# Kernel optimization log

Hardware: AMD Instinct MI355X
Metric: run time of the kernel (lower is better)

## Reference

```python
import jax, jax.numpy as jnp
import numpy as np

B, N, F = 32, 64, 128          # batch, num_nodes, n_in_node
K, H, M, NH = 4, 256, 256, 256 # edge_types, msg_hid, msg_out, n_hid
E = N * (N - 1)                # fully-connected directed edges = 4032


def setup_inputs() -> dict:
    key = jax.random.key(0)
    ks = jax.random.split(key, 12)
    inputs = jax.random.normal(ks[0], (B, N, F), dtype=jnp.float32)
    # soft edge-type assignment per edge (rows sum to 1, as in NRI)
    rel_type = jax.nn.softmax(jax.random.normal(ks[1], (B, E, K), dtype=jnp.float32), axis=-1)
    # one-hot receiver/sender matrices for all i != j pairs
    idx = np.array([(i, j) for i in range(N) for j in range(N) if i != j], dtype=np.int64)
    eye = np.eye(N, dtype=np.float32)
    rel_rec = jnp.asarray(eye[idx[:, 0]])   # [E, N]
    rel_send = jnp.asarray(eye[idx[:, 1]])  # [E, N]
    # per-edge-type message MLP weights (stacked over K): y = x @ W + b
    W1 = jax.random.normal(ks[2], (K, 2 * F, H), dtype=jnp.float32) / np.sqrt(2 * F)
    b1 = jnp.zeros((K, H), dtype=jnp.float32)
    W2 = jax.random.normal(ks[3], (K, H, M), dtype=jnp.float32) / np.sqrt(H)
    b2 = jnp.zeros((K, M), dtype=jnp.float32)
    # output MLP
    Wo1 = jax.random.normal(ks[4], (F + M, NH), dtype=jnp.float32) / np.sqrt(F + M)
    bo1 = jnp.zeros((NH,), dtype=jnp.float32)
    Wo2 = jax.random.normal(ks[5], (NH, NH), dtype=jnp.float32) / np.sqrt(NH)
    bo2 = jnp.zeros((NH,), dtype=jnp.float32)
    Wo3 = jax.random.normal(ks[6], (NH, F), dtype=jnp.float32) / np.sqrt(NH)
    bo3 = jnp.zeros((F,), dtype=jnp.float32)
    return {"inputs": inputs, "rel_type": rel_type, "rel_rec": rel_rec, "rel_send": rel_send,
            "W1": W1, "b1": b1, "W2": W2, "b2": b2,
            "Wo1": Wo1, "bo1": bo1, "Wo2": Wo2, "bo2": bo2, "Wo3": Wo3, "bo3": bo3}


def reference(inputs, rel_type, rel_rec, rel_send, W1, b1, W2, b2, Wo1, bo1, Wo2, bo2, Wo3, bo3):
    # gather node states to edges via one-hot matmul (as in the source)
    receivers = jnp.einsum('en,bnf->bef', rel_rec, inputs)   # [B,E,F]
    senders = jnp.einsum('en,bnf->bef', rel_send, inputs)    # [B,E,F]
    pre_msg = jnp.concatenate([receivers, senders], axis=-1)  # [B,E,2F]
    # per-edge-type 2-layer ReLU MLP, batched over the K edge types
    h = jax.nn.relu(jnp.einsum('bef,kfh->bkeh', pre_msg, W1) + b1[:, None, :])  # [B,K,E,H]
    msg = jax.nn.relu(jnp.einsum('bkeh,khm->bkem', h, W2) + b2[:, None, :])     # [B,K,E,M]
    # mask by soft edge type and accumulate over types (dropout p=0 -> identity)
    all_msgs = jnp.einsum('bkem,bek->bem', msg, rel_type)     # [B,E,M]
    # scatter-aggregate messages to receiver nodes via one-hot matmul
    agg_msgs = jnp.einsum('en,bem->bnm', rel_rec, all_msgs)   # [B,N,M]
    aug = jnp.concatenate([inputs, agg_msgs], axis=-1)        # [B,N,F+M]
    p = jax.nn.relu(aug @ Wo1 + bo1)
    p = jax.nn.relu(p @ Wo2 + bo2)
    p = p @ Wo3 + bo3
    return inputs + p
```

## Files before the change

### kernel.cpp

```cpp
#include <hip/hip_runtime.h>


#define B_ 32
#define N_ 64
#define F_ 128
#define K_ 4
#define E_ 4032

#define WS_W2T 0u
#define WS_R   524288u
#define WS_S   4718592u
#define WS_AGG 8912896u

typedef unsigned short u16;
typedef u16    u16x4  __attribute__((ext_vector_type(4)));
typedef u16    u16x8  __attribute__((ext_vector_type(8)));
typedef __bf16 bf16x8 __attribute__((ext_vector_type(8)));
typedef float  f32x4  __attribute__((ext_vector_type(4)));
typedef float  f32x16 __attribute__((ext_vector_type(16)));

__device__ __forceinline__ u16 f2bf(float f) {
    unsigned u; __builtin_memcpy(&u, &f, 4);
    return (u16)((u + 0x7FFFu + ((u >> 16) & 1u)) >> 16);
}
__device__ __forceinline__ float bf2f(u16 u) {
    unsigned v = ((unsigned)u) << 16;
    float f; __builtin_memcpy(&f, &v, 4); return f;
}
__device__ __forceinline__ void gl_lds16(const u16* g, u16* l) {
    __builtin_amdgcn_global_load_lds(
        (const __attribute__((address_space(1))) void*)g,
        (__attribute__((address_space(3))) void*)l, 16, 0, 0);
}

#define LBAR() do { \
    asm volatile("s_waitcnt lgkmcnt(0)" ::: "memory"); \
    __builtin_amdgcn_s_barrier(); \
    __builtin_amdgcn_sched_barrier(0); \
} while (0)

__global__ __launch_bounds__(256) void prep_rs_kernel(
    const float* __restrict__ W2, const float* __restrict__ x,
    const float* __restrict__ W1, const float* __restrict__ b1,
    u16* __restrict__ W2t, u16* __restrict__ R, u16* __restrict__ S)
{
    __shared__ u16 ldsA[64 * 136];
    __shared__ u16 ldsW[32 * 136];
    const int tid = threadIdx.x;

    if (blockIdx.x < 1024) {
        unsigned gid = blockIdx.x * 256u + tid;
        unsigned chunk = gid >> 13, r = gid & 8191u;
        unsigned g = r >> 11, n = (r >> 3) & 255u, e = r & 7u;
        unsigned k = chunk >> 3, kc = chunk & 7u, ks2 = g >> 1, lhh = g & 1u;
        unsigned kk = kc * 32u + ks2 * 16u + lhh * 8u + e;
        W2t[gid] = f2bf(W2[(k * 256u + kk) * 256u + n]);
        return;
    }

    const int lane = tid & 63, w = tid >> 6;
    const int quad = lane >> 4, mloc = lane & 15;
    const int bx = blockIdx.x - 1024;
    const int k = bx >> 6, half = (bx >> 5) & 1, b = bx & 31;

    for (int idx = tid; idx < 2048; idx += 256) {
        int row = idx >> 5, c4 = idx & 31;
        f32x4 v = *(const f32x4*)&x[(b * 64 + row) * 128 + c4 * 4];
        u16x4 o;
#pragma unroll
        for (int e = 0; e < 4; ++e) o[e] = f2bf(v[e]);
        *(u16x4*)&ldsA[row * 136 + c4 * 4] = o;
    }
    __syncthreads();

    bf16x8 aF[4];
#pragma unroll
    for (int ks = 0; ks < 4; ++ks)
        aF[ks] = *(const bf16x8*)&ldsA[(w * 16 + mloc) * 136 + quad * 8 + ks * 32];

    u16* dst = half ? S : R;
    for (int c = 0; c < 8; ++c) {
        __syncthreads();
        for (int idx = tid; idx < 4096; idx += 256) {
            int n = idx & 31, f = idx >> 5;
            ldsW[n * 136 + f] = f2bf(W1[(k * 256 + half * 128 + f) * 256 + c * 32 + n]);
        }
        __syncthreads();
#pragma unroll
        for (int nt = 0; nt < 2; ++nt) {
            f32x4 acc = (f32x4){0.f, 0.f, 0.f, 0.f};
            const int boff = (nt * 16 + mloc) * 136 + quad * 8;
#pragma unroll
            for (int ks = 0; ks < 4; ++ks)
                acc = __builtin_amdgcn_mfma_f32_16x16x32_bf16(
                    aF[ks], *(const bf16x8*)&ldsW[boff + ks * 32], acc, 0, 0, 0);
            const int n = c * 32 + nt * 16 + mloc;
            const float bias = half ? 0.f : b1[k * 256 + n];
#pragma unroll
            for (int r = 0; r < 4; ++r) {
                int row = w * 16 + quad * 4 + r;
                if (half) {
                    dst[((size_t)((k * 8 + c) * 2048 + b * 64 + row)) * 32 + nt * 16 + mloc]
                        = f2bf(acc[r] + bias);
                } else {
                    dst[((size_t)(k * 2048 + b * 64 + row)) * 256 + n] = f2bf(acc[r] + bias);
                }
            }
        }
    }
}

__global__ __launch_bounds__(256, 3) void edge9_kernel(
    const u16* __restrict__ R, const u16* __restrict__ S2,
    const float* __restrict__ rel, const u16* __restrict__ W2t,
    const float* __restrict__ b2, u16* __restrict__ aggb)
{
    __shared__ u16   WtS[2][8192];
    __shared__ u16   HS[2][4][64][8];
    __shared__ float Rf[4][256];
    __shared__ float rtS[4][64];

    const int tid  = threadIdx.x;
    const int lane = tid & 63;
    const int w    = tid >> 6;
    const int l31  = lane & 31;
    const int lh   = lane >> 5;
    const int bid  = ((blockIdx.x & 7) << 8) | (blockIdx.x >> 3);
    const int b    = bid >> 6;
    const int i    = bid & 63;

    {
        const u16* src = W2t + w * 2048;
        u16* dst = &WtS[0][w * 2048];
#pragma unroll
        for (int it2 = 0; it2 < 4; ++it2)
            gl_lds16(src + it2 * 512 + lane * 8, dst + it2 * 512);
    }
    {
        const int k = tid >> 6, j = tid & 63;
        float v = 0.f;
        if (j != i) v = rel[((size_t)(b * E_) + i * 63 + (j - (j > i))) * 4 + k];
        rtS[k][j] = v;
    }
    {
        const int k = tid >> 6, e4 = tid & 63;
        u16x4 t4 = *(const u16x4*)&R[((size_t)(k * 2048 + b * 64 + i)) * 256 + e4 * 4];
#pragma unroll
        for (int e = 0; e < 4; ++e) Rf[k][e4 * 4 + e] = bf2f(t4[e]);
    }
    u16x8 sv = *(const u16x8*)&S2[((size_t)(b * 64 + lane)) * 32 + w * 8];
    __syncthreads();

    {
        const float* rp = &Rf[0][w * 8];
        f32x4 r0 = *(const f32x4*)rp, r1 = *(const f32x4*)(rp + 4);
        bf16x8 o;
#pragma unroll
        for (int e = 0; e < 4; ++e) {
            o[e]     = (__bf16)fmaxf(r0[e] + bf2f(sv[e]),     0.f);
            o[4 + e] = (__bf16)fmaxf(r1[e] + bf2f(sv[4 + e]), 0.f);
        }
        *(bf16x8*)&HS[0][w][lane][0] = o;
    }
    __syncthreads();

    float amsg[2] = {0.f, 0.f};
    f32x16 acc[2][2];

    for (int it = 0; it < 32; ++it) {
        const int kT = it >> 3, kcT = it & 7;
        if (kcT == 0) {
#pragma unroll
            for (int mt = 0; mt < 2; ++mt)
#pragma unroll
                for (int nt = 0; nt < 2; ++nt) acc[mt][nt] = (f32x16)(0.f);
        }
        u16x8 svN;
        if (it < 31) {
            svN = *(const u16x8*)&S2[((size_t)((it + 1) * 2048 + b * 64 + lane)) * 32 + w * 8];
            const u16* src = W2t + (size_t)(it + 1) * 8192 + w * 2048;
            u16* dst = &WtS[(it + 1) & 1][w * 2048];
#pragma unroll
            for (int it2 = 0; it2 < 4; ++it2)
                gl_lds16(src + it2 * 512 + lane * 8, dst + it2 * 512);
        }
        const u16* buf = WtS[it & 1];
        const u16(*hs)[64][8] = HS[it & 1];
#pragma unroll
        for (int ks2 = 0; ks2 < 2; ++ks2) {
            bf16x8 A0 = *(const bf16x8*)&hs[ks2 * 2 + lh][l31][0];
            bf16x8 A1 = *(const bf16x8*)&hs[ks2 * 2 + lh][32 + l31][0];
            bf16x8 B0 = *(const bf16x8*)&buf[(ks2 * 2 + lh) * 2048 + (w * 64 + l31) * 8];
            bf16x8 B1 = *(const bf16x8*)&buf[(ks2 * 2 + lh) * 2048 + (w * 64 + 32 + l31) * 8];
            acc[0][0] = __builtin_amdgcn_mfma_f32_32x32x16_bf16(A0, B0, acc[0][0], 0, 0, 0);
            acc[0][1] = __builtin_amdgcn_mfma_f32_32x32x16_bf16(A0, B1, acc[0][1], 0, 0, 0);
            acc[1][0] = __builtin_amdgcn_mfma_f32_32x32x16_bf16(A1, B0, acc[1][0], 0, 0, 0);
            acc[1][1] = __builtin_amdgcn_mfma_f32_32x32x16_bf16(A1, B1, acc[1][1], 0, 0, 0);
        }
        if (it < 31) {
            const int kT2 = (it + 1) >> 3, kc2 = (it + 1) & 7;
            const float* rp = &Rf[kT2][kc2 * 32 + w * 8];
            f32x4 r0 = *(const f32x4*)rp, r1 = *(const f32x4*)(rp + 4);
            bf16x8 o;
#pragma unroll
            for (int e = 0; e < 4; ++e) {
                o[e]     = (__bf16)fmaxf(r0[e] + bf2f(svN[e]),     0.f);
                o[4 + e] = (__bf16)fmaxf(r1[e] + bf2f(svN[4 + e]), 0.f);
            }
            *(bf16x8*)&HS[(it + 1) & 1][w][lane][0] = o;
        }
        if (kcT == 7) {
#pragma unroll
            for (int nt = 0; nt < 2; ++nt) {
                const float bias = b2[kT * 256 + w * 64 + nt * 32 + l31];
#pragma unroll
                for (int mt = 0; mt < 2; ++mt) {
                    float s = 0.f;
#pragma unroll
                    for (int rq = 0; rq < 4; ++rq) {
                        f32x4 rt4 = *(const f32x4*)&rtS[kT][mt * 32 + rq * 8 + 4 * lh];
#pragma unroll
                        for (int e = 0; e < 4; ++e) {
                            float v = acc[mt][nt][rq * 4 + e] + bias;
                            v = v > 0.f ? v : 0.f;
                            s += rt4[e] * v;
                        }
                    }
                    amsg[nt] += s;
                }
            }
        }
        __syncthreads();
    }

#pragma unroll
    for (int nt = 0; nt < 2; ++nt) {
        float s = amsg[nt] + __shfl_xor(amsg[nt], 32);
        if (lh == 0)
            aggb[(size_t)(b * 64 + i) * 256 + w * 64 + nt * 32 + l31] = f2bf(s);
    }
}

__global__ __launch_bounds__(256) void outmlp3_kernel(
    const float* __restrict__ x, const u16* __restrict__ aggb,
    const float* __restrict__ Wo1, const float* __restrict__ bo1,
    const float* __restrict__ Wo2, const float* __restrict__ bo2,
    const float* __restrict__ Wo3, const float* __restrict__ bo3,
    float* __restrict__ out)
{
    __shared__ u16 wch[4][256][8];
    __shared__ u16 p1S[32 * 264];
    __shared__ u16 p2S[32 * 264];
    const int tid = threadIdx.x, lane = tid & 63, w = tid >> 6;
    const int quad = lane >> 4, mloc = lane & 15;
    const int row0 = blockIdx.x * 32;

    {
        f32x4 acc[2][4];
#pragma unroll
        for (int mt = 0; mt < 2; ++mt)
#pragma unroll
            for (int nt = 0; nt < 4; ++nt) acc[mt][nt] = (f32x4){0.f, 0.f, 0.f, 0.f};
        float wr[32];
#pragma unroll
        for (int g = 0; g < 4; ++g)
#pragma unroll
            for (int e = 0; e < 8; ++e) wr[g * 8 + e] = Wo1[(g * 8 + e) * 256 + tid];
        for (int kk = 0; kk < 12; ++kk) {
            bf16x8 aF[2];
#pragma unroll
            for (int mt = 0; mt < 2; ++mt) {
                const int row = row0 + mt * 16 + mloc;
                if (kk < 4) {
                    u16x8 t;
#pragma unroll
                    for (int e = 0; e < 8; ++e) t[e] = f2bf(x[row * 128 + kk * 32 + quad * 8 + e]);
                    __builtin_memcpy(&aF[mt], &t, 16);
                } else {
                    aF[mt] = *(const bf16x8*)&aggb[(size_t)row * 256 + (kk - 4) * 32 + quad * 8];
                }
            }
#pragma unroll
            for (int g = 0; g < 4; ++g) {
                u16x8 o;
#pragma unroll
                for (int e = 0; e < 8; ++e) o[e] = f2bf(wr[g * 8 + e]);
                *(u16x8*)&wch[g][tid][0] = o;
            }
            if (kk + 1 < 12) {
#pragma unroll
                for (int g = 0; g < 4; ++g)
#pragma unroll
                    for (int e = 0; e < 8; ++e) wr[g * 8 + e] = Wo1[((kk + 1) * 32 + g * 8 + e) * 256 + tid];
            }
            LBAR();
#pragma unroll
            for (int nt = 0; nt < 4; ++nt) {
                bf16x8 bF = *(const bf16x8*)&wch[quad][w * 64 + nt * 16 + mloc][0];
#pragma unroll
                for (int mt = 0; mt < 2; ++mt)
                    acc[mt][nt] = __builtin_amdgcn_mfma_f32_16x16x32_bf16(aF[mt], bF, acc[mt][nt], 0, 0, 0);
            }
            LBAR();
        }
#pragma unroll
        for (int nt = 0; nt < 4; ++nt) {
            const int n = w * 64 + nt * 16 + mloc;
            const float bias = bo1[n];
#pragma unroll
            for (int mt = 0; mt < 2; ++mt)
#pragma unroll
                for (int r = 0; r < 4; ++r) {
                    float v = acc[mt][nt][r] + bias;
                    p1S[(mt * 16 + quad * 4 + r) * 264 + n] = f2bf(v > 0.f ? v : 0.f);
                }
        }
    }
    LBAR();
    {
        f32x4 acc[2][4];
#pragma unroll
        for (int mt = 0; mt < 2; ++mt)
#pragma unroll
            for (int nt = 0; nt < 4; ++nt) acc[mt][nt] = (f32x4){0.f, 0.f, 0.f, 0.f};
        float wr[32];
#pragma unroll
        for (int g = 0; g < 4; ++g)
#pragma unroll
            for (int e = 0; e < 8; ++e) wr[g * 8 + e] = Wo2[(g * 8 + e) * 256 + tid];
        for (int kk = 0; kk < 8; ++kk) {
            bf16x8 aF[2];
#pragma unroll
            for (int mt = 0; mt < 2; ++mt)
                aF[mt] = *(const bf16x8*)&p1S[(mt * 16 + mloc) * 264 + kk * 32 + quad * 8];
#pragma unroll
            for (int g = 0; g < 4; ++g) {
                u16x8 o;
#pragma unroll
                for (int e = 0; e < 8; ++e) o[e] = f2bf(wr[g * 8 + e]);
                *(u16x8*)&wch[g][tid][0] = o;
            }
            if (kk + 1 < 8) {
#pragma unroll
                for (int g = 0; g < 4; ++g)
#pragma unroll
                    for (int e = 0; e < 8; ++e) wr[g * 8 + e] = Wo2[((kk + 1) * 32 + g * 8 + e) * 256 + tid];
            }
            LBAR();
#pragma unroll
            for (int nt = 0; nt < 4; ++nt) {
                bf16x8 bF = *(const bf16x8*)&wch[quad][w * 64 + nt * 16 + mloc][0];
#pragma unroll
                for (int mt = 0; mt < 2; ++mt)
                    acc[mt][nt] = __builtin_amdgcn_mfma_f32_16x16x32_bf16(aF[mt], bF, acc[mt][nt], 0, 0, 0);
            }
            LBAR();
        }
#pragma unroll
        for (int nt = 0; nt < 4; ++nt) {
            const int n = w * 64 + nt * 16 + mloc;
            const float bias = bo2[n];
#pragma unroll
            for (int mt = 0; mt < 2; ++mt)
#pragma unroll
                for (int r = 0; r < 4; ++r) {
                    float v = acc[mt][nt][r] + bias;
                    p2S[(mt * 16 + quad * 4 + r) * 264 + n] = f2bf(v > 0.f ? v : 0.f);
                }
        }
    }
    LBAR();
    {
        f32x4 acc[2][2];
#pragma unroll
        for (int mt = 0; mt < 2; ++mt)
#pragma unroll
            for (int nt = 0; nt < 2; ++nt) acc[mt][nt] = (f32x4){0.f, 0.f, 0.f, 0.f};
        const int sn = tid & 127, sh = tid >> 7;
        float wr[16];
#pragma unroll
        for (int g2 = 0; g2 < 2; ++g2)
#pragma unroll
            for (int e = 0; e < 8; ++e) wr[g2 * 8 + e] = Wo3[((sh * 2 + g2) * 8 + e) * 128 + sn];
        for (int kk = 0; kk < 8; ++kk) {
            bf16x8 aF[2];
#pragma unroll
            for (int mt = 0; mt < 2; ++mt)
                aF[mt] = *(const bf16x8*)&p2S[(mt * 16 + mloc) * 264 + kk * 32 + quad * 8];
#pragma unroll
            for (int g2 = 0; g2 < 2; ++g2) {
                const int g = sh * 2 + g2;
                u16x8 o;
#pragma unroll
                for (int e = 0; e < 8; ++e) o[e] = f2bf(wr[g2 * 8 + e]);
                *(u16x8*)&wch[g][sn][0] = o;
            }
            if (kk + 1 < 8) {
#pragma unroll
                for (int g2 = 0; g2 < 2; ++g2)
#pragma unroll
                    for (int e = 0; e < 8; ++e)
                        wr[g2 * 8 + e] = Wo3[((kk + 1) * 32 + (sh * 2 + g2) * 8 + e) * 128 + sn];
            }
            LBAR();
#pragma unroll
            for (int nt = 0; nt < 2; ++nt) {
                bf16x8 bF = *(const bf16x8*)&wch[quad][w * 32 + nt * 16 + mloc][0];
#pragma unroll
                for (int mt = 0; mt < 2; ++mt)
                    acc[mt][nt] = __builtin_amdgcn_mfma_f32_16x16x32_bf16(aF[mt], bF, acc[mt][nt], 0, 0, 0);
            }
            LBAR();
        }
#pragma unroll
        for (int nt = 0; nt < 2; ++nt) {
            const int n = w * 32 + nt * 16 + mloc;
            const float bias = bo3[n];
#pragma unroll
            for (int mt = 0; mt < 2; ++mt)
#pragma unroll
                for (int r = 0; r < 4; ++r) {
                    const int grow = row0 + mt * 16 + quad * 4 + r;
                    out[grow * 128 + n] = x[grow * 128 + n] + acc[mt][nt][r] + bias;
                }
        }
    }
}

extern "C" void kernel_launch(void* const* d_in, const int* in_sizes, int n_in,
                              void* d_out, int out_size, void* d_ws, size_t ws_size,
                              hipStream_t stream) {
    const float* x   = (const float*)d_in[0];
    const float* rel = (const float*)d_in[1];
    const float* W1  = (const float*)d_in[4];
    const float* b1  = (const float*)d_in[5];
    const float* W2  = (const float*)d_in[6];
    const float* b2  = (const float*)d_in[7];
    const float* Wo1 = (const float*)d_in[8];
    const float* bo1 = (const float*)d_in[9];
    const float* Wo2 = (const float*)d_in[10];
    const float* bo2 = (const float*)d_in[11];
    const float* Wo3 = (const float*)d_in[12];
    const float* bo3 = (const float*)d_in[13];
    float* out = (float*)d_out;

    char* ws = (char*)d_ws;
    u16* W2t  = (u16*)(ws + WS_W2T);
    u16* R    = (u16*)(ws + WS_R);
    u16* S2   = (u16*)(ws + WS_S);
    u16* aggb = (u16*)(ws + WS_AGG);

    prep_rs_kernel<<<1280, 256, 0, stream>>>(W2, x, W1, b1, W2t, R, S2);
    edge9_kernel<<<2048, 256, 0, stream>>>(R, S2, rel, W2t, b2, aggb);
    outmlp3_kernel<<<64, 256, 0, stream>>>(x, aggb, Wo1, bo1, Wo2, bo2, Wo3, bo3, out);
}
```

Before: 224.6 us.

## Load MFMA operands directly from global memory, dropping LDS staging and barriers

The edge kernel stops staging W2 tiles and hidden activations through double-buffered LDS with a barrier on every iteration. Each lane now loads its B fragments of W2t and its sender rows straight from global memory into registers, and builds the A operands in registers. The inner loop is fully unrolled per edge type. This removes LDS traffic and 32 block syncs per block but depends on L1/L2 caching of W2t and S2, with more global loads and higher register pressure.

```diff
diff --git a/kernel.cpp b/kernel.cpp
--- a/kernel.cpp
+++ b/kernel.cpp
@@ -26,11 +26,6 @@
 __device__ __forceinline__ float bf2f(u16 u) {
     unsigned v = ((unsigned)u) << 16;
     float f; __builtin_memcpy(&f, &v, 4); return f;
-}
-__device__ __forceinline__ void gl_lds16(const u16* g, u16* l) {
-    __builtin_amdgcn_global_load_lds(
-        (const __attribute__((address_space(1))) void*)g,
-        (__attribute__((address_space(3))) void*)l, 16, 0, 0);
 }
 
 #define LBAR() do { \
@@ -110,13 +105,11 @@
     }
 }
 
-__global__ __launch_bounds__(256, 3) void edge9_kernel(
+__global__ __launch_bounds__(256, 3) void edge10_kernel(
     const u16* __restrict__ R, const u16* __restrict__ S2,
     const float* __restrict__ rel, const u16* __restrict__ W2t,
     const float* __restrict__ b2, u16* __restrict__ aggb)
 {
-    __shared__ u16   WtS[2][8192];
-    __shared__ u16   HS[2][4][64][8];
     __shared__ float Rf[4][256];
     __shared__ float rtS[4][64];
 
@@ -130,13 +123,6 @@
     const int i    = bid & 63;
 
     {
-        const u16* src = W2t + w * 2048;
-        u16* dst = &WtS[0][w * 2048];
-#pragma unroll
-        for (int it2 = 0; it2 < 4; ++it2)
-            gl_lds16(src + it2 * 512 + lane * 8, dst + it2 * 512);
-    }
-    {
         const int k = tid >> 6, j = tid & 63;
         float v = 0.f;
         if (j != i) v = rel[((size_t)(b * E_) + i * 63 + (j - (j > i))) * 4 + k];
@@ -148,89 +134,67 @@
 #pragma unroll
         for (int e = 0; e < 4; ++e) Rf[k][e4 * 4 + e] = bf2f(t4[e]);
     }
-    u16x8 sv = *(const u16x8*)&S2[((size_t)(b * 64 + lane)) * 32 + w * 8];
     __syncthreads();
 
-    {
-        const float* rp = &Rf[0][w * 8];
-        f32x4 r0 = *(const f32x4*)rp, r1 = *(const f32x4*)(rp + 4);
-        bf16x8 o;
-#pragma unroll
-        for (int e = 0; e < 4; ++e) {
-            o[e]     = (__bf16)fmaxf(r0[e] + bf2f(sv[e]),     0.f);
-            o[4 + e] = (__bf16)fmaxf(r1[e] + bf2f(sv[4 + e]), 0.f);
-        }
-        *(bf16x8*)&HS[0][w][lane][0] = o;
-    }
-    __syncthreads();
+    const u16* Sb0 = S2 + (size_t)(b * 64 + l31) * 32 + lh * 8;
+    const u16* Sb1 = S2 + (size_t)(b * 64 + 32 + l31) * 32 + lh * 8;
+    const u16* Wb  = W2t + lh * 2048 + (w * 64 + l31) * 8;
 
     float amsg[2] = {0.f, 0.f};
-    f32x16 acc[2][2];
-
-    for (int it = 0; it < 32; ++it) {
-        const int kT = it >> 3, kcT = it & 7;
-        if (kcT == 0) {
-#pragma unroll
-            for (int mt = 0; mt < 2; ++mt)
-#pragma unroll
-                for (int nt = 0; nt < 2; ++nt) acc[mt][nt] = (f32x16)(0.f);
-        }
-        u16x8 svN;
-        if (it < 31) {
-            svN = *(const u16x8*)&S2[((size_t)((it + 1) * 2048 + b * 64 + lane)) * 32 + w * 8];
-            const u16* src = W2t + (size_t)(it + 1) * 8192 + w * 2048;
-            u16* dst = &WtS[(it + 1) & 1][w * 2048];
-#pragma unroll
-            for (int it2 = 0; it2 < 4; ++it2)
-                gl_lds16(src + it2 * 512 + lane * 8, dst + it2 * 512);
-        }
-        const u16* buf = WtS[it & 1];
-        const u16(*hs)[64][8] = HS[it & 1];
-#pragma unroll
-        for (int ks2 = 0; ks2 < 2; ++ks2) {
-            bf16x8 A0 = *(const bf16x8*)&hs[ks2 * 2 + lh][l31][0];
-            bf16x8 A1 = *(const bf16x8*)&hs[ks2 * 2 + lh][32 + l31][0];
-            bf16x8 B0 = *(const bf16x8*)&buf[(ks2 * 2 + lh) * 2048 + (w * 64 + l31) * 8];
-            bf16x8 B1 = *(const bf16x8*)&buf[(ks2 * 2 + lh) * 2048 + (w * 64 + 32 + l31) * 8];
-            acc[0][0] = __builtin_amdgcn_mfma_f32_32x32x16_bf16(A0, B0, acc[0][0], 0, 0, 0);
-            acc[0][1] = __builtin_amdgcn_mfma_f32_32x32x16_bf16(A0, B1, acc[0][1], 0, 0, 0);
-            acc[1][0] = __builtin_amdgcn_mfma_f32_32x32x16_bf16(A1, B0, acc[1][0], 0, 0, 0);
-            acc[1][1] = __builtin_amdgcn_mfma_f32_32x32x16_bf16(A1, B1, acc[1][1], 0, 0, 0);
-        }
-        if (it < 31) {
-            const int kT2 = (it + 1) >> 3, kc2 = (it + 1) & 7;
-            const float* rp = &Rf[kT2][kc2 * 32 + w * 8];
-            f32x4 r0 = *(const f32x4*)rp, r1 = *(const f32x4*)(rp + 4);
-            bf16x8 o;
-#pragma unroll
-            for (int e = 0; e < 4; ++e) {
-                o[e]     = (__bf16)fmaxf(r0[e] + bf2f(svN[e]),     0.f);
-                o[4 + e] = (__bf16)fmaxf(r1[e] + bf2f(svN[4 + e]), 0.f);
-            }
-            *(bf16x8*)&HS[(it + 1) & 1][w][lane][0] = o;
-        }
-        if (kcT == 7) {
-#pragma unroll
-            for (int nt = 0; nt < 2; ++nt) {
-                const float bias = b2[kT * 256 + w * 64 + nt * 32 + l31];
-#pragma unroll
-                for (int mt = 0; mt < 2; ++mt) {
-                    float s = 0.f;
-#pragma unroll
-                    for (int rq = 0; rq < 4; ++rq) {
-                        f32x4 rt4 = *(const f32x4*)&rtS[kT][mt * 32 + rq * 8 + 4 * lh];
-#pragma unroll
-                        for (int e = 0; e < 4; ++e) {
-                            float v = acc[mt][nt][rq * 4 + e] + bias;
-                            v = v > 0.f ? v : 0.f;
-                            s += rt4[e] * v;
-                        }
+
+    for (int kT = 0; kT < 4; ++kT) {
+        f32x16 acc[2][2];
+#pragma unroll
+        for (int mt = 0; mt < 2; ++mt)
+#pragma unroll
+            for (int nt = 0; nt < 2; ++nt) acc[mt][nt] = (f32x16)(0.f);
+
+#pragma unroll
+        for (int kc = 0; kc < 8; ++kc) {
+            const int it = kT * 8 + kc;
+#pragma unroll
+            for (int ks2 = 0; ks2 < 2; ++ks2) {
+                u16x8 s0 = *(const u16x8*)(Sb0 + (size_t)it * 65536 + ks2 * 16);
+                u16x8 s1 = *(const u16x8*)(Sb1 + (size_t)it * 65536 + ks2 * 16);
+                const float* rp = &Rf[kT][kc * 32 + ks2 * 16 + lh * 8];
+                f32x4 r0 = *(const f32x4*)rp, r1 = *(const f32x4*)(rp + 4);
+                bf16x8 A0, A1;
+#pragma unroll
+                for (int e = 0; e < 4; ++e) {
+                    A0[e]     = (__bf16)fmaxf(r0[e] + bf2f(s0[e]),     0.f);
+                    A0[4 + e] = (__bf16)fmaxf(r1[e] + bf2f(s0[4 + e]), 0.f);
+                    A1[e]     = (__bf16)fmaxf(r0[e] + bf2f(s1[e]),     0.f);
+                    A1[4 + e] = (__bf16)fmaxf(r1[e] + bf2f(s1[4 + e]), 0.f);
+                }
+                const u16* wp = Wb + (size_t)it * 8192 + ks2 * 4096;
+                bf16x8 B0 = *(const bf16x8*)(wp);
+                bf16x8 B1 = *(const bf16x8*)(wp + 256);
+                acc[0][0] = __builtin_amdgcn_mfma_f32_32x32x16_bf16(A0, B0, acc[0][0], 0, 0, 0);
+                acc[0][1] = __builtin_amdgcn_mfma_f32_32x32x16_bf16(A0, B1, acc[0][1], 0, 0, 0);
+                acc[1][0] = __builtin_amdgcn_mfma_f32_32x32x16_bf16(A1, B0, acc[1][0], 0, 0, 0);
+                acc[1][1] = __builtin_amdgcn_mfma_f32_32x32x16_bf16(A1, B1, acc[1][1], 0, 0, 0);
+            }
+        }
+
+#pragma unroll
+        for (int nt = 0; nt < 2; ++nt) {
+            const float bias = b2[kT * 256 + w * 64 + nt * 32 + l31];
+#pragma unroll
+            for (int mt = 0; mt < 2; ++mt) {
+                float s = 0.f;
+#pragma unroll
+                for (int rq = 0; rq < 4; ++rq) {
+                    f32x4 rt4 = *(const f32x4*)&rtS[kT][mt * 32 + rq * 8 + 4 * lh];
+#pragma unroll
+                    for (int e = 0; e < 4; ++e) {
+                        float v = acc[mt][nt][rq * 4 + e] + bias;
+                        v = v > 0.f ? v : 0.f;
+                        s += rt4[e] * v;
                     }
-                    amsg[nt] += s;
-                }
-            }
-        }
-        __syncthreads();
+                }
+                amsg[nt] += s;
+            }
+        }
     }
 
 #pragma unroll
@@ -451,6 +415,6 @@
     u16* aggb = (u16*)(ws + WS_AGG);
 
     prep_rs_kernel<<<1280, 256, 0, stream>>>(W2, x, W1, b1, W2t, R, S2);
-    edge9_kernel<<<2048, 256, 0, stream>>>(R, S2, rel, W2t, b2, aggb);
+    edge10_kernel<<<2048, 256, 0, stream>>>(R, S2, rel, W2t, b2, aggb);
     outmlp3_kernel<<<64, 256, 0, stream>>>(x, aggb, Wo1, bo1, Wo2, bo2, Wo3, bo3, out);
 }
```

Result: no change. 228.6 us (+1.8%).
